# Performance work log

Hardware: AMD Instinct MI355X
Metric: run time of the kernel (lower is better)

The kernel has to match this reference:

```python
import jax, jax.numpy as jnp
import numpy as np

B, S, D = 4, 1024, 1024
H = 16
HD = D // H  # head_dim = 64


def setup_inputs() -> dict:
    key = jax.random.key(0)
    k1, k2, k3 = jax.random.split(key, 3)
    x = jax.random.normal(k1, (B, S, D), dtype=jnp.float32)
    # qkv_proj: Linear(input_dim, 3*embed_dim), stored as (in, out) for x @ W
    scale = 1.0 / np.sqrt(D)
    W_qkv = jax.random.uniform(k2, (D, 3 * D), dtype=jnp.float32, minval=-scale, maxval=scale)
    b_qkv = jax.random.uniform(k3, (3 * D,), dtype=jnp.float32, minval=-scale, maxval=scale)
    return {"x": x, "W_qkv": W_qkv, "b_qkv": b_qkv}


def reference(x, W_qkv, b_qkv):
    b, s, _ = x.shape
    qkv = x @ W_qkv + b_qkv                       # [B,S,3D]
    qkv = qkv.reshape(b, s, H, 3 * HD)            # [B,S,H,3*hd]
    qkv = qkv.transpose(0, 2, 1, 3)               # [B,H,S,3*hd]
    q, k, v = jnp.split(qkv, 3, axis=-1)          # each [B,H,S,hd]
    scores = jnp.einsum('bhqd,bhkd->bhqk', q, k) / jnp.sqrt(jnp.float32(HD))
    attn = jax.nn.softmax(scores, axis=-1)        # [B,H,S,S]
    out = jnp.einsum('bhqk,bhkd->bhqd', attn, v)  # [B,H,S,hd]
    values = out.transpose(0, 2, 1, 3).reshape(b, s, H * HD)  # [B,S,D]
    return values
```

## Files before the change

### kernel.cpp

```cpp
#include <hip/hip_runtime.h>
#include <hip/hip_bf16.h>
#include <stdint.h>

#define BATCH 4
#define SEQ 1024
#define DMODEL 1024
#define NH 16
#define HD 64

typedef __attribute__((ext_vector_type(8))) short short8;
typedef __attribute__((ext_vector_type(4))) float f32x4;

__device__ __forceinline__ unsigned short f2bf(float f) {
    union { float f; uint32_t u; } v; v.f = f;
    uint32_t r = v.u + 0x7fff + ((v.u >> 16) & 1);
    return (unsigned short)(r >> 16);
}

__device__ __forceinline__ uint32_t pack2bf(float lo, float hi) {
    return (uint32_t)f2bf(lo) | ((uint32_t)f2bf(hi) << 16);
}

__device__ __forceinline__ void async_copy16(const unsigned short* g, unsigned short* l) {
    __builtin_amdgcn_global_load_lds(
        (__attribute__((address_space(1))) void*)g,
        (__attribute__((address_space(3))) void*)l,
        16, 0, 0);
}

__global__ __launch_bounds__(256) void cast_x_kernel(const float* __restrict__ x,
                                                     unsigned short* __restrict__ xb) {
    int t = blockIdx.x * 256 + threadIdx.x;
    const float4* p = (const float4*)x + (size_t)t * 2;
    float4 a = p[0], b = p[1];
    short8 o;
    o[0] = (short)f2bf(a.x); o[1] = (short)f2bf(a.y);
    o[2] = (short)f2bf(a.z); o[3] = (short)f2bf(a.w);
    o[4] = (short)f2bf(b.x); o[5] = (short)f2bf(b.y);
    o[6] = (short)f2bf(b.z); o[7] = (short)f2bf(b.w);
    *((short8*)xb + t) = o;
}

__global__ __launch_bounds__(256) void transpose_w_kernel(const float* __restrict__ W,
                                                          unsigned short* __restrict__ Wt) {
    __shared__ float tile[32][33];
    int tx = threadIdx.x & 31;
    int ty = threadIdx.x >> 5;
    int nb = blockIdx.x * 32;
    int kb = blockIdx.y * 32;
#pragma unroll
    for (int i = 0; i < 4; i++) {
        int k = kb + ty + i * 8;
        tile[ty + i * 8][tx] = W[(size_t)k * 3072 + nb + tx];
    }
    __syncthreads();
#pragma unroll
    for (int i = 0; i < 4; i++) {
        int n = nb + ty + i * 8;
        Wt[(size_t)n * 1024 + kb + tx] = f2bf(tile[tx][ty + i * 8]);
    }
}

#define BM 128
#define BN 128
#define BKK 64

__global__ __launch_bounds__(256) void qkv_gemm_kernel(
    const unsigned short* __restrict__ xb,
    const unsigned short* __restrict__ wt,
    const float* __restrict__ bias,
    unsigned short* __restrict__ Qb,
    unsigned short* __restrict__ Kb,
    unsigned short* __restrict__ VbT)
{
    __shared__ __align__(16) unsigned short As[BM][64];
    __shared__ __align__(16) unsigned short Bs[BN][64];
    int tid = threadIdx.x;
    int wave = tid >> 6, lane = tid & 63;
    int quad = lane >> 4, l16 = lane & 15;
    int wm = wave >> 1, wn = wave & 1;
    int m0 = blockIdx.x * BM;
    int n0 = blockIdx.y * BN;

    int grow = lane >> 3;
    int gcol = ((lane & 7) ^ grow) << 3;
    const unsigned short* gA = xb + (size_t)(m0 + wave * 32 + grow) * 1024 + gcol;
    const unsigned short* gB = wt + (size_t)(n0 + wave * 32 + grow) * 1024 + gcol;
    unsigned short* ldsA = &As[wave * 32][0];
    unsigned short* ldsB = &Bs[wave * 32][0];
    int sw = l16 & 7;

    f32x4 acc[4][4] = {};
    for (int k0 = 0; k0 < 1024; k0 += BKK) {
        __syncthreads();
#pragma unroll
        for (int i = 0; i < 4; i++) {
            async_copy16(gA + (size_t)i * 8 * 1024 + k0, ldsA + i * 512);
            async_copy16(gB + (size_t)i * 8 * 1024 + k0, ldsB + i * 512);
        }
        __syncthreads();
#pragma unroll
        for (int kk = 0; kk < BKK; kk += 32) {
            int kb = kk >> 3;
            short8 af[4], bf[4];
#pragma unroll
            for (int t = 0; t < 4; t++) {
                int ar = wm * 64 + t * 16 + l16;
                af[t] = *(const short8*)&As[ar][((kb + quad) ^ sw) << 3];
            }
#pragma unroll
            for (int t = 0; t < 4; t++) {
                int br = wn * 64 + t * 16 + l16;
                bf[t] = *(const short8*)&Bs[br][((kb + quad) ^ sw) << 3];
            }
#pragma unroll
            for (int mt = 0; mt < 4; mt++)
#pragma unroll
                for (int nt = 0; nt < 4; nt++)
                    acc[mt][nt] = __builtin_amdgcn_mfma_f32_16x16x32_bf16(
                        af[mt], bf[nt], acc[mt][nt], 0, 0, 0);
        }
    }
#pragma unroll
    for (int nt = 0; nt < 4; nt++) {
        int n = n0 + wn * 64 + nt * 16 + l16;
        int h = n / 192;
        int c = n - h * 192;
        int which = c >> 6;
        int d = c & 63;
        float bv = bias[n];
        float sc = (which == 0) ? 0.125f : 1.0f;
#pragma unroll
        for (int mt = 0; mt < 4; mt++) {
#pragma unroll
            for (int r = 0; r < 4; r++) {
                int m = m0 + wm * 64 + mt * 16 + quad * 4 + r;
                int b = m >> 10, s = m & 1023;
                float v = (acc[mt][nt][r] + bv) * sc;
                unsigned short bf_v = f2bf(v);
                int bh = b * 16 + h;
                if (which == 2) {
                    VbT[((size_t)bh * 64 + d) * 1024 + s] = bf_v;
                } else {
                    unsigned short* dst = (which == 0) ? Qb : Kb;
                    dst[((size_t)bh * 1024 + s) * 64 + d] = bf_v;
                }
            }
        }
    }
}

#define BQ 64
#define BKV 128
#define LDQ 72
#define LDP 136

__global__ __launch_bounds__(256, 3) void attn_kernel(
    const unsigned short* __restrict__ Qb,
    const unsigned short* __restrict__ Kb,
    const unsigned short* __restrict__ VbT,
    float* __restrict__ out)
{
    __shared__ unsigned short Qs[BQ][LDQ];
    __shared__ unsigned short Ks[BKV][LDQ];
    __shared__ unsigned short Vts[HD][LDP];

    int tid = threadIdx.x;
    int wave = tid >> 6, lane = tid & 63;
    int quad = lane >> 4, l16 = lane & 15;
    int bh = blockIdx.y;
    int q0 = blockIdx.x * BQ;
    const unsigned short* Qp = Qb + (size_t)bh * SEQ * HD;
    const unsigned short* Kp = Kb + (size_t)bh * SEQ * HD;
    const unsigned short* Vp = VbT + (size_t)bh * HD * SEQ;

#pragma unroll
    for (int i = 0; i < 2; i++) {
        int chunk = tid + i * 256;
        int row = chunk >> 3, c8 = (chunk & 7) * 8;
        *(short8*)&Qs[row][c8] = *(const short8*)&Qp[(size_t)(q0 + row) * HD + c8];
    }

    f32x4 oacc[4] = {};
    float lsum = 0.f;

    int srcA = ((lane & 16) << 1) | l16;
    int srcB = srcA + 16;
    bool hiQ = (lane & 32) != 0;

    for (int kt = 0; kt < SEQ; kt += BKV) {
        __syncthreads();
#pragma unroll
        for (int i = 0; i < 4; i++) {
            int chunk = tid + i * 256;
            int krow = chunk >> 3, kc8 = (chunk & 7) * 8;
            *(short8*)&Ks[krow][kc8] = *(const short8*)&Kp[(size_t)(kt + krow) * HD + kc8];
            int vrow = chunk >> 4, vc8 = (chunk & 15) * 8;
            *(short8*)&Vts[vrow][vc8] = *(const short8*)&Vp[(size_t)vrow * SEQ + kt + vc8];
        }
        __syncthreads();

        f32x4 sacc[8] = {};
#pragma unroll
        for (int ds_ = 0; ds_ < HD; ds_ += 32) {
            short8 qf = *(const short8*)&Qs[wave * 16 + l16][ds_ + quad * 8];
            short8 kf[8];
#pragma unroll
            for (int nt = 0; nt < 8; nt++)
                kf[nt] = *(const short8*)&Ks[nt * 16 + l16][ds_ + quad * 8];
#pragma unroll
            for (int nt = 0; nt < 8; nt++)
                sacc[nt] = __builtin_amdgcn_mfma_f32_16x16x32_bf16(kf[nt], qf, sacc[nt], 0, 0, 0);
        }

        uint32_t u[8][2];
#pragma unroll
        for (int nt = 0; nt < 8; nt++) {
            float p0 = __expf(sacc[nt][0]);
            float p1 = __expf(sacc[nt][1]);
            float p2 = __expf(sacc[nt][2]);
            float p3 = __expf(sacc[nt][3]);
            lsum += (p0 + p1) + (p2 + p3);
            u[nt][0] = pack2bf(p0, p1);
            u[nt][1] = pack2bf(p2, p3);
        }

#pragma unroll
        for (int kb4 = 0; kb4 < 4; kb4++) {
            int tA = kb4 * 2, tB = tA + 1;
            uint32_t w0a = (uint32_t)__shfl((int)u[tA][0], srcA, 64);
            uint32_t w1a = (uint32_t)__shfl((int)u[tA][1], srcA, 64);
            uint32_t w2a = (uint32_t)__shfl((int)u[tA][0], srcB, 64);
            uint32_t w3a = (uint32_t)__shfl((int)u[tA][1], srcB, 64);
            uint32_t w0b = (uint32_t)__shfl((int)u[tB][0], srcA, 64);
            uint32_t w1b = (uint32_t)__shfl((int)u[tB][1], srcA, 64);
            uint32_t w2b = (uint32_t)__shfl((int)u[tB][0], srcB, 64);
            uint32_t w3b = (uint32_t)__shfl((int)u[tB][1], srcB, 64);
            union { uint32_t w[4]; short8 s; } pf;
            pf.w[0] = hiQ ? w0b : w0a;
            pf.w[1] = hiQ ? w1b : w1a;
            pf.w[2] = hiQ ? w2b : w2a;
            pf.w[3] = hiQ ? w3b : w3a;
#pragma unroll
            for (int nt = 0; nt < 4; nt++) {
                short8 vf = *(const short8*)&Vts[nt * 16 + l16][kb4 * 32 + quad * 8];
                oacc[nt] = __builtin_amdgcn_mfma_f32_16x16x32_bf16(vf, pf.s, oacc[nt], 0, 0, 0);
            }
        }
    }

    lsum += __shfl_xor(lsum, 16, 64);
    lsum += __shfl_xor(lsum, 32, 64);
    float inv = 1.f / lsum;

    int b = bh >> 4, h = bh & 15;
    int s = q0 + wave * 16 + l16;
#pragma unroll
    for (int nt = 0; nt < 4; nt++) {
        float4 o;
        o.x = oacc[nt][0] * inv;
        o.y = oacc[nt][1] * inv;
        o.z = oacc[nt][2] * inv;
        o.w = oacc[nt][3] * inv;
        *(float4*)&out[(size_t)(b * SEQ + s) * DMODEL + h * HD + nt * 16 + quad * 4] = o;
    }
}

extern "C" void kernel_launch(void* const* d_in, const int* in_sizes, int n_in,
                              void* d_out, int out_size, void* d_ws, size_t ws_size,
                              hipStream_t stream) {
    const float* x    = (const float*)d_in[0];
    const float* W    = (const float*)d_in[1];
    const float* bias = (const float*)d_in[2];
    float* out = (float*)d_out;
    char* ws = (char*)d_ws;

    unsigned short* xb  = (unsigned short*)(ws);
    unsigned short* wt  = (unsigned short*)(ws + 8388608);
    unsigned short* Qb  = (unsigned short*)(ws + 14680064);
    unsigned short* Kb  = (unsigned short*)(ws + 23068672);
    unsigned short* VbT = (unsigned short*)(ws + 31457280);

    cast_x_kernel<<<2048, 256, 0, stream>>>(x, xb);
    dim3 tg(96, 32);
    transpose_w_kernel<<<tg, 256, 0, stream>>>(W, wt);
    dim3 gg(32, 24);
    qkv_gemm_kernel<<<gg, 256, 0, stream>>>(xb, wt, bias, Qb, Kb, VbT);
    dim3 ag(SEQ / BQ, BATCH * NH);
    attn_kernel<<<ag, 256, 0, stream>>>(Qb, Kb, VbT, out);
}
```

Measured before the change: 166.9 us.

## Fuse prep kernels and restructure attention with larger Q tile, swizzled LDS, XCD mapping

Merges the x cast and W transpose into one launch, removing a kernel launch. The attention kernel now handles 128 queries per block, with two 16-row groups per wave that share each K and V fragment load. Padded shared memory is replaced by XOR-swizzled layouts. The K rows are permuted so the exp'd scores map directly onto the PV MFMA operand without cross-lane shuffles. Blocks are remapped so heads group by XCD, which should help L2 reuse of K/V, at the cost of more registers and lower occupancy (2 blocks per CU).

New measurement: 159.1 us. -4.7%, faster.

```diff
diff --git a/kernel.cpp b/kernel.cpp
--- a/kernel.cpp
+++ b/kernel.cpp
@@ -28,36 +28,39 @@
         16, 0, 0);
 }
 
-__global__ __launch_bounds__(256) void cast_x_kernel(const float* __restrict__ x,
-                                                     unsigned short* __restrict__ xb) {
-    int t = blockIdx.x * 256 + threadIdx.x;
-    const float4* p = (const float4*)x + (size_t)t * 2;
-    float4 a = p[0], b = p[1];
-    short8 o;
-    o[0] = (short)f2bf(a.x); o[1] = (short)f2bf(a.y);
-    o[2] = (short)f2bf(a.z); o[3] = (short)f2bf(a.w);
-    o[4] = (short)f2bf(b.x); o[5] = (short)f2bf(b.y);
-    o[6] = (short)f2bf(b.z); o[7] = (short)f2bf(b.w);
-    *((short8*)xb + t) = o;
-}
-
-__global__ __launch_bounds__(256) void transpose_w_kernel(const float* __restrict__ W,
-                                                          unsigned short* __restrict__ Wt) {
+__global__ __launch_bounds__(256) void prep_kernel(const float* __restrict__ x,
+                                                   const float* __restrict__ W,
+                                                   unsigned short* __restrict__ xb,
+                                                   unsigned short* __restrict__ Wt) {
     __shared__ float tile[32][33];
-    int tx = threadIdx.x & 31;
-    int ty = threadIdx.x >> 5;
-    int nb = blockIdx.x * 32;
-    int kb = blockIdx.y * 32;
-#pragma unroll
-    for (int i = 0; i < 4; i++) {
-        int k = kb + ty + i * 8;
-        tile[ty + i * 8][tx] = W[(size_t)k * 3072 + nb + tx];
-    }
-    __syncthreads();
-#pragma unroll
-    for (int i = 0; i < 4; i++) {
-        int n = nb + ty + i * 8;
-        Wt[(size_t)n * 1024 + kb + tx] = f2bf(tile[tx][ty + i * 8]);
+    int bid = blockIdx.x;
+    if (bid < 2048) {
+        int t = bid * 256 + threadIdx.x;
+        const float4* p = (const float4*)x + (size_t)t * 2;
+        float4 a = p[0], b = p[1];
+        short8 o;
+        o[0] = (short)f2bf(a.x); o[1] = (short)f2bf(a.y);
+        o[2] = (short)f2bf(a.z); o[3] = (short)f2bf(a.w);
+        o[4] = (short)f2bf(b.x); o[5] = (short)f2bf(b.y);
+        o[6] = (short)f2bf(b.z); o[7] = (short)f2bf(b.w);
+        *((short8*)xb + t) = o;
+    } else {
+        int r = bid - 2048;
+        int nb = (r % 96) * 32;
+        int kb = (r / 96) * 32;
+        int tx = threadIdx.x & 31;
+        int ty = threadIdx.x >> 5;
+#pragma unroll
+        for (int i = 0; i < 4; i++) {
+            int k = kb + ty + i * 8;
+            tile[ty + i * 8][tx] = W[(size_t)k * 3072 + nb + tx];
+        }
+        __syncthreads();
+#pragma unroll
+        for (int i = 0; i < 4; i++) {
+            int n = nb + ty + i * 8;
+            Wt[(size_t)n * 1024 + kb + tx] = f2bf(tile[tx][ty + i * 8]);
+        }
     }
 }
 
@@ -150,119 +153,137 @@
     }
 }
 
-#define BQ 64
+#define BQ 128
 #define BKV 128
-#define LDQ 72
-#define LDP 136
-
-__global__ __launch_bounds__(256, 3) void attn_kernel(
+
+__global__ __launch_bounds__(256, 2) void attn_kernel(
     const unsigned short* __restrict__ Qb,
     const unsigned short* __restrict__ Kb,
     const unsigned short* __restrict__ VbT,
     float* __restrict__ out)
 {
-    __shared__ unsigned short Qs[BQ][LDQ];
-    __shared__ unsigned short Ks[BKV][LDQ];
-    __shared__ unsigned short Vts[HD][LDP];
+    __shared__ unsigned short Qs[BQ][64];
+    __shared__ unsigned short Ks[BKV][64];
+    __shared__ unsigned short Vts[HD][128];
 
     int tid = threadIdx.x;
     int wave = tid >> 6, lane = tid & 63;
     int quad = lane >> 4, l16 = lane & 15;
-    int bh = blockIdx.y;
-    int q0 = blockIdx.x * BQ;
+
+    int id = blockIdx.x;
+    int xcd = id & 7, rest = id >> 3;
+    int qt = rest & 7, grp = rest >> 3;
+    int bh = grp * 8 + xcd;
+    int q0 = qt * BQ;
+
     const unsigned short* Qp = Qb + (size_t)bh * SEQ * HD;
     const unsigned short* Kp = Kb + (size_t)bh * SEQ * HD;
     const unsigned short* Vp = VbT + (size_t)bh * HD * SEQ;
 
-#pragma unroll
-    for (int i = 0; i < 2; i++) {
-        int chunk = tid + i * 256;
-        int row = chunk >> 3, c8 = (chunk & 7) * 8;
-        *(short8*)&Qs[row][c8] = *(const short8*)&Qp[(size_t)(q0 + row) * HD + c8];
-    }
-
-    f32x4 oacc[4] = {};
-    float lsum = 0.f;
-
-    int srcA = ((lane & 16) << 1) | l16;
-    int srcB = srcA + 16;
-    bool hiQ = (lane & 32) != 0;
+    int f_q = (l16 & 3) | (((l16 >> 3) & 1) << 2);
+    int f_k = (l16 & 3) | (((l16 >> 2) & 1) << 2);
+    int f_v = l16 & 7;
+    int rbase = ((l16 >> 2) << 3) | (l16 & 3);
+
+#pragma unroll
+    for (int i = 0; i < 4; i++) {
+        int idx = i * 256 + tid;
+        int row = idx >> 3, pb = idx & 7;
+        int fr = (row & 3) | (((row >> 3) & 1) << 2);
+        int lb = pb ^ fr;
+        *(short8*)&Qs[row][pb * 8] = *(const short8*)&Qp[(size_t)(q0 + row) * HD + lb * 8];
+    }
+
+    f32x4 oacc[2][4] = {};
+    float lsum[2] = {0.f, 0.f};
 
     for (int kt = 0; kt < SEQ; kt += BKV) {
         __syncthreads();
 #pragma unroll
         for (int i = 0; i < 4; i++) {
-            int chunk = tid + i * 256;
-            int krow = chunk >> 3, kc8 = (chunk & 7) * 8;
-            *(short8*)&Ks[krow][kc8] = *(const short8*)&Kp[(size_t)(kt + krow) * HD + kc8];
-            int vrow = chunk >> 4, vc8 = (chunk & 15) * 8;
-            *(short8*)&Vts[vrow][vc8] = *(const short8*)&Vp[(size_t)vrow * SEQ + kt + vc8];
-        }
-        __syncthreads();
-
-        f32x4 sacc[8] = {};
+            int idx = i * 256 + tid;
+            int krow = idx >> 3, kpb = idx & 7;
+            int kfr = (krow & 3) | (((krow >> 3) & 1) << 2);
+            int klb = kpb ^ kfr;
+            *(short8*)&Ks[krow][kpb * 8] = *(const short8*)&Kp[(size_t)(kt + krow) * HD + klb * 8];
+            int vrow = idx >> 4, vpb = idx & 15;
+            int vlb = vpb ^ (vrow & 7);
+            *(short8*)&Vts[vrow][vpb * 8] = *(const short8*)&Vp[(size_t)vrow * SEQ + kt + vlb * 8];
+        }
+        __syncthreads();
+
+        f32x4 sacc[2][8] = {};
 #pragma unroll
         for (int ds_ = 0; ds_ < HD; ds_ += 32) {
-            short8 qf = *(const short8*)&Qs[wave * 16 + l16][ds_ + quad * 8];
-            short8 kf[8];
-#pragma unroll
-            for (int nt = 0; nt < 8; nt++)
-                kf[nt] = *(const short8*)&Ks[nt * 16 + l16][ds_ + quad * 8];
-#pragma unroll
-            for (int nt = 0; nt < 8; nt++)
-                sacc[nt] = __builtin_amdgcn_mfma_f32_16x16x32_bf16(kf[nt], qf, sacc[nt], 0, 0, 0);
-        }
-
-        uint32_t u[8][2];
-#pragma unroll
-        for (int nt = 0; nt < 8; nt++) {
-            float p0 = __expf(sacc[nt][0]);
-            float p1 = __expf(sacc[nt][1]);
-            float p2 = __expf(sacc[nt][2]);
-            float p3 = __expf(sacc[nt][3]);
-            lsum += (p0 + p1) + (p2 + p3);
-            u[nt][0] = pack2bf(p0, p1);
-            u[nt][1] = pack2bf(p2, p3);
-        }
-
-#pragma unroll
-        for (int kb4 = 0; kb4 < 4; kb4++) {
-            int tA = kb4 * 2, tB = tA + 1;
-            uint32_t w0a = (uint32_t)__shfl((int)u[tA][0], srcA, 64);
-            uint32_t w1a = (uint32_t)__shfl((int)u[tA][1], srcA, 64);
-            uint32_t w2a = (uint32_t)__shfl((int)u[tA][0], srcB, 64);
-            uint32_t w3a = (uint32_t)__shfl((int)u[tA][1], srcB, 64);
-            uint32_t w0b = (uint32_t)__shfl((int)u[tB][0], srcA, 64);
-            uint32_t w1b = (uint32_t)__shfl((int)u[tB][1], srcA, 64);
-            uint32_t w2b = (uint32_t)__shfl((int)u[tB][0], srcB, 64);
-            uint32_t w3b = (uint32_t)__shfl((int)u[tB][1], srcB, 64);
-            union { uint32_t w[4]; short8 s; } pf;
-            pf.w[0] = hiQ ? w0b : w0a;
-            pf.w[1] = hiQ ? w1b : w1a;
-            pf.w[2] = hiQ ? w2b : w2a;
-            pf.w[3] = hiQ ? w3b : w3a;
-#pragma unroll
-            for (int nt = 0; nt < 4; nt++) {
-                short8 vf = *(const short8*)&Vts[nt * 16 + l16][kb4 * 32 + quad * 8];
-                oacc[nt] = __builtin_amdgcn_mfma_f32_16x16x32_bf16(vf, pf.s, oacc[nt], 0, 0, 0);
-            }
-        }
-    }
-
-    lsum += __shfl_xor(lsum, 16, 64);
-    lsum += __shfl_xor(lsum, 32, 64);
-    float inv = 1.f / lsum;
+            int k0b = ds_ >> 3;
+            short8 qf[2];
+#pragma unroll
+            for (int g = 0; g < 2; g++)
+                qf[g] = *(const short8*)&Qs[wave * 32 + g * 16 + l16][((k0b + quad) ^ f_q) * 8];
+#pragma unroll
+            for (int nt = 0; nt < 8; nt++) {
+                int krow = rbase + ((nt >> 1) << 5) + ((nt & 1) << 2);
+                short8 kf = *(const short8*)&Ks[krow][((k0b + quad) ^ f_k) * 8];
+#pragma unroll
+                for (int g = 0; g < 2; g++)
+                    sacc[g][nt] = __builtin_amdgcn_mfma_f32_16x16x32_bf16(kf, qf[g], sacc[g][nt], 0, 0, 0);
+            }
+        }
+
+        uint32_t u[2][8][2];
+#pragma unroll
+        for (int g = 0; g < 2; g++)
+#pragma unroll
+            for (int nt = 0; nt < 8; nt++) {
+                float p0 = __expf(sacc[g][nt][0]);
+                float p1 = __expf(sacc[g][nt][1]);
+                float p2 = __expf(sacc[g][nt][2]);
+                float p3 = __expf(sacc[g][nt][3]);
+                lsum[g] += (p0 + p1) + (p2 + p3);
+                u[g][nt][0] = pack2bf(p0, p1);
+                u[g][nt][1] = pack2bf(p2, p3);
+            }
+
+#pragma unroll
+        for (int c = 0; c < 4; c++) {
+            short8 vf[4];
+#pragma unroll
+            for (int nt = 0; nt < 4; nt++)
+                vf[nt] = *(const short8*)&Vts[nt * 16 + l16][(((c << 2) + quad) ^ f_v) * 8];
+#pragma unroll
+            for (int g = 0; g < 2; g++) {
+                union { uint32_t w[4]; short8 s; } pf;
+                pf.w[0] = u[g][2 * c][0];
+                pf.w[1] = u[g][2 * c][1];
+                pf.w[2] = u[g][2 * c + 1][0];
+                pf.w[3] = u[g][2 * c + 1][1];
+#pragma unroll
+                for (int nt = 0; nt < 4; nt++)
+                    oacc[g][nt] = __builtin_amdgcn_mfma_f32_16x16x32_bf16(vf[nt], pf.s, oacc[g][nt], 0, 0, 0);
+            }
+        }
+    }
+
+#pragma unroll
+    for (int g = 0; g < 2; g++) {
+        lsum[g] += __shfl_xor(lsum[g], 16, 64);
+        lsum[g] += __shfl_xor(lsum[g], 32, 64);
+    }
 
     int b = bh >> 4, h = bh & 15;
-    int s = q0 + wave * 16 + l16;
-#pragma unroll
-    for (int nt = 0; nt < 4; nt++) {
-        float4 o;
-        o.x = oacc[nt][0] * inv;
-        o.y = oacc[nt][1] * inv;
-        o.z = oacc[nt][2] * inv;
-        o.w = oacc[nt][3] * inv;
-        *(float4*)&out[(size_t)(b * SEQ + s) * DMODEL + h * HD + nt * 16 + quad * 4] = o;
+#pragma unroll
+    for (int g = 0; g < 2; g++) {
+        float inv = 1.f / lsum[g];
+        int s = q0 + wave * 32 + g * 16 + l16;
+#pragma unroll
+        for (int nt = 0; nt < 4; nt++) {
+            float4 o;
+            o.x = oacc[g][nt][0] * inv;
+            o.y = oacc[g][nt][1] * inv;
+            o.z = oacc[g][nt][2] * inv;
+            o.w = oacc[g][nt][3] * inv;
+            *(float4*)&out[(size_t)(b * SEQ + s) * DMODEL + h * HD + nt * 16 + quad * 4] = o;
+        }
     }
 }
 
@@ -281,11 +302,8 @@
     unsigned short* Kb  = (unsigned short*)(ws + 23068672);
     unsigned short* VbT = (unsigned short*)(ws + 31457280);
 
-    cast_x_kernel<<<2048, 256, 0, stream>>>(x, xb);
-    dim3 tg(96, 32);
-    transpose_w_kernel<<<tg, 256, 0, stream>>>(W, wt);
+    prep_kernel<<<5120, 256, 0, stream>>>(x, W, xb, wt);
     dim3 gg(32, 24);
     qkv_gemm_kernel<<<gg, 256, 0, stream>>>(xb, wt, bias, Qb, Kb, VbT);
-    dim3 ag(SEQ / BQ, BATCH * NH);
-    attn_kernel<<<ag, 256, 0, stream>>>(Qb, Kb, VbT, out);
-}
+    attn_kernel<<<512, 256, 0, stream>>>(Qb, Kb, VbT, out);
+}
```
